# Optimization experiments

Measured on AMD Instinct MI355X. Metric: run time of the kernel, lower is better.

## Reference

```python
import jax, jax.numpy as jnp
import numpy as np

B, H, W, DIM, NH = 2, 48, 48, 768, 12
HD = DIM // NH  # 64


def setup_inputs() -> dict:
    key = jax.random.key(0)
    ks = jax.random.split(key, 7)
    std = 0.02
    return {
        "x": jax.random.normal(ks[0], (B, H, W, DIM), jnp.float32),
        "rel_pos_h": jax.random.normal(ks[1], (2 * H - 1, HD), jnp.float32) * std,
        "rel_pos_w": jax.random.normal(ks[2], (2 * W - 1, HD), jnp.float32) * std,
        "qkv_w": jax.random.normal(ks[3], (3 * DIM, DIM), jnp.float32) * std,
        "qkv_b": jnp.zeros((3 * DIM,), jnp.float32),
        "proj_w": jax.random.normal(ks[4], (DIM, DIM), jnp.float32) * std,
        "proj_b": jnp.zeros((DIM,), jnp.float32),
    }


def reference(x, rel_pos_h, rel_pos_w, qkv_w, qkv_b, proj_w, proj_b):
    b, h, w, dim = x.shape
    nh = NH
    hd = dim // nh
    scale = hd ** -0.5
    n = h * w
    # qkv projection: (B,N,3*dim) -> (3, B*nh, N, hd)
    qkv = x.reshape(b, n, dim) @ qkv_w.T + qkv_b
    qkv = qkv.reshape(b, n, 3, nh, hd).transpose(2, 0, 3, 1, 4).reshape(3, b * nh, n, hd)
    q, k, v = qkv[0], qkv[1], qkv[2]
    # scaled dot-product scores (B*nh, N, N)
    attn = jnp.einsum('bnc,bmc->bnm', q * scale, k)
    # decomposed relative position bias (q_size == k_size, no interpolation)
    idx_h = jnp.arange(h)[:, None] - jnp.arange(h)[None, :] + (h - 1)  # (h,h)
    idx_w = jnp.arange(w)[:, None] - jnp.arange(w)[None, :] + (w - 1)  # (w,w)
    Rh = rel_pos_h[idx_h]  # (h, h, hd)
    Rw = rel_pos_w[idx_w]  # (w, w, hd)
    r_q = q.reshape(b * nh, h, w, hd)
    rel_h = jnp.einsum('bhwc,hkc->bhwk', r_q, Rh)  # (B*nh, h, w, h)
    rel_w = jnp.einsum('bhwc,wkc->bhwk', r_q, Rw)  # (B*nh, h, w, w)
    attn = (attn.reshape(b * nh, h, w, h, w)
            + rel_h[:, :, :, :, None]
            + rel_w[:, :, :, None, :]).reshape(b * nh, n, n)
    attn = jax.nn.softmax(attn, axis=-1)
    out = (attn @ v).reshape(b, nh, h, w, hd).transpose(0, 2, 3, 1, 4).reshape(b, h, w, dim)
    return out @ proj_w.T + proj_b
```

## Files before the change

kernel.cpp:

```cpp
#include <hip/hip_runtime.h>
#include <hip/hip_bf16.h>
#include <stdint.h>

#define NQ    2304
#define MROWS 4608
#define DIMC  768
#define NHEAD 12
#define HEADS 24
#define HD    64

typedef unsigned int uint;
typedef unsigned short u16;
typedef __attribute__((ext_vector_type(8))) short s16x8;
typedef __attribute__((ext_vector_type(4))) float f32x4;

#define MFMA16(a, b, c) __builtin_amdgcn_mfma_f32_16x16x32_bf16((a), (b), (c), 0, 0, 0)

static __device__ __forceinline__ float bfbits2f(uint u) {
  union { uint i; float f; } c; c.i = u << 16; return c.f;
}
static __device__ __forceinline__ u16 f2bf(float f) {
  __hip_bfloat16 h = __float2bfloat16(f);
  union { __hip_bfloat16 h; u16 u; } c; c.h = h; return c.u;
}
static __device__ __forceinline__ u16 f2h(float f) {
  union { _Float16 h; u16 u; } c; c.h = (_Float16)f; return c.u;
}
static __device__ __forceinline__ float h2f(u16 u) {
  union { u16 u; _Float16 h; } c; c.u = u; return (float)c.h;
}
static __device__ __forceinline__ void dec8(uint4 p, float* f) {
  f[0] = bfbits2f(p.x & 0xFFFFu); f[1] = bfbits2f(p.x >> 16);
  f[2] = bfbits2f(p.y & 0xFFFFu); f[3] = bfbits2f(p.y >> 16);
  f[4] = bfbits2f(p.z & 0xFFFFu); f[5] = bfbits2f(p.z >> 16);
  f[6] = bfbits2f(p.w & 0xFFFFu); f[7] = bfbits2f(p.w >> 16);
}
static __device__ __forceinline__ void ld8(const void* p, size_t idx, int bf, float* f) {
  if (bf) { dec8(*(const uint4*)((const u16*)p + idx), f); }
  else {
    const float4* q = (const float4*)((const float*)p + idx);
    float4 a = q[0], b = q[1];
    f[0] = a.x; f[1] = a.y; f[2] = a.z; f[3] = a.w;
    f[4] = b.x; f[5] = b.y; f[6] = b.z; f[7] = b.w;
  }
}
static __device__ __forceinline__ float ld1(const void* p, size_t idx, int bf) {
  return bf ? bfbits2f(((const u16*)p)[idx]) : ((const float*)p)[idx];
}
static __device__ __forceinline__ uint4 ld8_to_bf(const void* p, size_t idx, int bf) {
  if (bf) return *(const uint4*)((const u16*)p + idx);
  float f[8]; ld8(p, idx, 0, f);
  uint4 u;
  u.x = (uint)f2bf(f[0]) | ((uint)f2bf(f[1]) << 16);
  u.y = (uint)f2bf(f[2]) | ((uint)f2bf(f[3]) << 16);
  u.z = (uint)f2bf(f[4]) | ((uint)f2bf(f[5]) << 16);
  u.w = (uint)f2bf(f[6]) | ((uint)f2bf(f[7]) << 16);
  return u;
}
static __device__ __forceinline__ void gll16(const u16* g, u16* l) {
  __builtin_amdgcn_global_load_lds(
      (const __attribute__((address_space(1))) unsigned int*)g,
      (__attribute__((address_space(3))) unsigned int*)l, 16, 0, 0);
}

__global__ __launch_bounds__(256) void detect_k(const u16* __restrict__ x,
                                                int* __restrict__ mode) {
  __shared__ int wsum[4];
  int t = threadIdx.x;
  int cnt = 0;
  for (int i = 0; i < 8; ++i) {
    uint u = x[(size_t)(t * 8 + i) * 2];
    uint e = (u >> 7) & 0xFFu;
    uint mag = u & 0x7FFFu;
    if (mag == 0 || (e >= 113 && e <= 133)) cnt++;
  }
#pragma unroll
  for (int d = 1; d < 64; d <<= 1) cnt += __shfl_xor(cnt, d);
  if ((t & 63) == 0) wsum[t >> 6] = cnt;
  __syncthreads();
  if (t == 0) mode[0] = ((wsum[0] + wsum[1] + wsum[2] + wsum[3]) > 1024) ? 1 : 0;
}

#define NX8 442368u
#define NW8 221184u
#define NP8 73728u
__global__ __launch_bounds__(256) void convert_k(
    const void* __restrict__ x, const void* __restrict__ qkvw,
    const void* __restrict__ pw, const int* __restrict__ mode,
    u16* __restrict__ xb, u16* __restrict__ wb, u16* __restrict__ pwb)
{
  const int bf = mode[0];
  uint i8 = blockIdx.x * 256 + threadIdx.x;
  if (i8 < NX8) {
    *(uint4*)(xb + (size_t)i8 * 8) = ld8_to_bf(x, (size_t)i8 * 8, bf);
  } else if (i8 < NX8 + NW8) {
    size_t j = i8 - NX8;
    *(uint4*)(wb + j * 8) = ld8_to_bf(qkvw, j * 8, bf);
  } else if (i8 < NX8 + NW8 + NP8) {
    size_t j = i8 - NX8 - NW8;
    *(uint4*)(pwb + j * 8) = ld8_to_bf(pw, j * 8, bf);
  }
}

__global__ __launch_bounds__(256) void qkv_gemm_k(
    const u16* __restrict__ Xb, const u16* __restrict__ Wb,
    const void* __restrict__ Bq, const int* __restrict__ mode,
    u16* __restrict__ Q, u16* __restrict__ K, u16* __restrict__ Vt)
{
  __shared__ __align__(16) u16 As[128][32];
  __shared__ __align__(16) u16 Bs[128][32];
  __shared__ __align__(16) u16 Ts[128][72];
  const int bf = mode[0];
  const int t = threadIdx.x;
  const int w = t >> 6, lane = t & 63, l15 = t & 15, quad = (t >> 4) & 3;
  const int wr = w >> 1, wc = w & 1;
  const int row0 = blockIdx.y << 7, col0 = blockIdx.x << 7;
  const int r4 = lane >> 2, c8 = (lane & 3) << 3;

  f32x4 zero4 = {0.f, 0.f, 0.f, 0.f};
  f32x4 acc[4][4];
#pragma unroll
  for (int i = 0; i < 4; ++i)
#pragma unroll
    for (int j = 0; j < 4; ++j) acc[i][j] = zero4;

  for (int kt = 0; kt < DIMC; kt += 32) {
    __syncthreads();
    gll16(Xb + (size_t)(row0 + (w << 5) + r4) * DIMC + kt + c8,      &As[(w << 5)][0]);
    gll16(Xb + (size_t)(row0 + (w << 5) + 16 + r4) * DIMC + kt + c8, &As[(w << 5) + 16][0]);
    gll16(Wb + (size_t)(col0 + (w << 5) + r4) * DIMC + kt + c8,      &Bs[(w << 5)][0]);
    gll16(Wb + (size_t)(col0 + (w << 5) + 16 + r4) * DIMC + kt + c8, &Bs[(w << 5) + 16][0]);
    __syncthreads();
    s16x8 af[4], bfr[4];
#pragma unroll
    for (int i = 0; i < 4; ++i)
      af[i] = *(const s16x8*)&As[(wr << 6) + (i << 4) + l15][quad << 3];
#pragma unroll
    for (int j = 0; j < 4; ++j)
      bfr[j] = *(const s16x8*)&Bs[(wc << 6) + (j << 4) + l15][quad << 3];
#pragma unroll
    for (int i = 0; i < 4; ++i)
#pragma unroll
      for (int j = 0; j < 4; ++j)
        acc[i][j] = MFMA16(af[i], bfr[j], acc[i][j]);
  }

  if (blockIdx.x < 12) {
#pragma unroll
    for (int jt = 0; jt < 4; ++jt) {
      int col = col0 + (wc << 6) + (jt << 4) + l15;
      int which = col / DIMC;
      int rem = col - which * DIMC;
      int head = rem >> 6, d = rem & 63;
      float bv = ld1(Bq, col, bf);
      u16* dst = (which == 0) ? Q : K;
#pragma unroll
      for (int i = 0; i < 4; ++i)
#pragma unroll
        for (int r = 0; r < 4; ++r) {
          int mrow = row0 + (wr << 6) + (i << 4) + (quad << 2) + r;
          int b_ = (mrow >= NQ) ? 1 : 0;
          int n = mrow - b_ * NQ;
          dst[(((size_t)(b_ * NHEAD + head)) * NQ + n) * HD + d] = f2bf(acc[i][jt][r] + bv);
        }
    }
  } else {
    int b_ = (row0 >= NQ) ? 1 : 0;
    int n0 = row0 - b_ * NQ;
#pragma unroll
    for (int h = 0; h < 2; ++h) {
      if (wc == h) {
#pragma unroll
        for (int jt = 0; jt < 4; ++jt) {
          int coll = (jt << 4) + l15;
          float bv = ld1(Bq, col0 + (h << 6) + coll, bf);
#pragma unroll
          for (int i = 0; i < 4; ++i)
#pragma unroll
            for (int r = 0; r < 4; ++r) {
              int tok = (wr << 6) + (i << 4) + (quad << 2) + r;
              Ts[tok][coll] = f2bf(acc[i][jt][r] + bv);
            }
        }
      }
      __syncthreads();
      int head = ((col0 - 1536) >> 6) + h;
      u16* dst = Vt + ((size_t)(b_ * NHEAD + head) * HD) * NQ + n0;
      int d = t >> 2, ch = (t & 3) << 5;
#pragma unroll
      for (int c4 = 0; c4 < 4; ++c4) {
        u16 tmp[8];
#pragma unroll
        for (int j = 0; j < 8; ++j) tmp[j] = Ts[ch + (c4 << 3) + j][d];
        *(uint4*)(dst + (size_t)d * NQ + ch + (c4 << 3)) = *(uint4*)tmp;
      }
      __syncthreads();
    }
  }
}

__global__ __launch_bounds__(256) void bias_gemm_k(
    const u16* __restrict__ Qw,
    const void* __restrict__ rph, const void* __restrict__ rpw,
    const int* __restrict__ mode,
    u16* __restrict__ Bh_g, u16* __restrict__ Bw_g)
{
  __shared__ __align__(16) u16 As[128][72];
  __shared__ __align__(16) u16 Bs[192][72];
  const int bf = mode[0];
  const int t = threadIdx.x;
  const int w = t >> 6, l15 = t & 15, quad = (t >> 4) & 3;
  const int wr = w >> 1, wc = w & 1;
  const int blk = blockIdx.x;
  const int bhd = blk / 18;
  const int row0 = (blk - bhd * 18) << 7;

  {
    int lr = t >> 1, lk = (t & 1) << 5;
    const u16* src = Qw + ((size_t)bhd * NQ + row0 + lr) * HD + lk;
    *(uint4*)&As[lr][lk]      = *(const uint4*)(src);
    *(uint4*)&As[lr][lk + 8]  = *(const uint4*)(src + 8);
    *(uint4*)&As[lr][lk + 16] = *(const uint4*)(src + 16);
    *(uint4*)&As[lr][lk + 24] = *(const uint4*)(src + 24);
  }
  for (int e = t; e < 384; e += 256) {
    int row = e >> 1, k32 = (e & 1) << 5;
    int tab = (row >= 96) ? 1 : 0;
    int r2 = row - (tab ? 96 : 0);
    if (r2 > 94) r2 = 0;
    const void* src = tab ? rpw : rph;
    *(uint4*)&Bs[row][k32]      = ld8_to_bf(src, (size_t)r2 * HD + k32, bf);
    *(uint4*)&Bs[row][k32 + 8]  = ld8_to_bf(src, (size_t)r2 * HD + k32 + 8, bf);
    *(uint4*)&Bs[row][k32 + 16] = ld8_to_bf(src, (size_t)r2 * HD + k32 + 16, bf);
    *(uint4*)&Bs[row][k32 + 24] = ld8_to_bf(src, (size_t)r2 * HD + k32 + 24, bf);
  }
  __syncthreads();

  f32x4 zero4 = {0.f, 0.f, 0.f, 0.f};
  f32x4 acc[4][6];
#pragma unroll
  for (int i = 0; i < 4; ++i)
#pragma unroll
    for (int j = 0; j < 6; ++j) acc[i][j] = zero4;

#pragma unroll
  for (int ks = 0; ks < 2; ++ks) {
    s16x8 af[4], bfr[6];
#pragma unroll
    for (int i = 0; i < 4; ++i)
      af[i] = *(const s16x8*)&As[(wr << 6) + (i << 4) + l15][(ks << 5) + (quad << 3)];
#pragma unroll
    for (int j = 0; j < 6; ++j)
      bfr[j] = *(const s16x8*)&Bs[wc * 96 + (j << 4) + l15][(ks << 5) + (quad << 3)];
#pragma unroll
    for (int i = 0; i < 4; ++i)
#pragma unroll
      for (int j = 0; j < 6; ++j)
        acc[i][j] = MFMA16(af[i], bfr[j], acc[i][j]);
  }

#pragma unroll
  for (int jt = 0; jt < 6; ++jt) {
    int col = wc * 96 + (jt << 4) + l15;
    int tab = (col >= 96) ? 1 : 0;
    int j = col - (tab ? 96 : 0);
    if (j >= 95) continue;
    u16* dstT = tab ? Bw_g : Bh_g;
#pragma unroll
    for (int i = 0; i < 4; ++i)
#pragma unroll
      for (int r = 0; r < 4; ++r) {
        int n = row0 + (wr << 6) + (i << 4) + (quad << 2) + r;
        int qh = (n * 10923) >> 19;
        int coord = tab ? (n - qh * 48) : qh;
        int c = coord + 47 - j;
        if (c >= 0 && c < 48)
          dstT[((size_t)bhd * 48 + c) * NQ + n] = f2h(acc[i][jt][r]);
      }
  }
}

#define ATILE(KB, KN, T0, PREF, KM) do {                                      \
    f32x4 acc_s[2][4];                                                        \
    _Pragma("unroll")                                                         \
    for (int nc = 0; nc < 4; ++nc) {                                          \
      f32x4 a0 = MFMA16(KB[2*nc], qa0[0], zero4);                             \
      acc_s[0][nc] = MFMA16(KB[2*nc+1], qa1[0], a0);                          \
      f32x4 a1 = MFMA16(KB[2*nc], qa0[1], zero4);                             \
      acc_s[1][nc] = MFMA16(KB[2*nc+1], qa1[1], a1);                          \
    }                                                                         \
    if (PREF) {                                                               \
      _Pragma("unroll")                                                       \
      for (int nc = 0; nc < 4; ++nc) {                                        \
        const u16* kp_ = kbase + (size_t)((T0) + 64 + (nc << 4) + l15) * HD + (quad << 3); \
        KN[2*nc]   = *(const s16x8*)(kp_);                                    \
        KN[2*nc+1] = *(const s16x8*)(kp_ + 32);                               \
      }                                                                       \
    }                                                                         \
    int kh0 = ((T0) * 10923) >> 19;                                           \
    int thr = (kh0 + 1) * 48 - (T0);                                          \
    uint Wq[2][8];                                                            \
    _Pragma("unroll")                                                         \
    for (int g = 0; g < 2; ++g) {                                             \
      int qrl = (w << 5) + (g << 4) + l15;                                    \
      float bh0v = h2f(BhL[kh0][qrl]);                                        \
      float bh1v = h2f(BhL[kh0 + 1][qrl]);                                    \
      float sum = 0.f;                                                        \
      _Pragma("unroll")                                                       \
      for (int nc = 0; nc < 4; ++nc) {                                        \
        int bnc = (KM) + (nc << 4);                                           \
        bnc = (bnc >= 48) ? bnc - 48 : bnc;                                   \
        uint2 pv = *(const uint2*)&BwL[qrl][bnc + (quad << 2)];               \
        float b0 = h2f((u16)(pv.x & 0xFFFFu));                                \
        float b1 = h2f((u16)(pv.x >> 16));                                    \
        float b2 = h2f((u16)(pv.y & 0xFFFFu));                                \
        float b3 = h2f((u16)(pv.y >> 16));                                    \
        int kl = (nc << 4) + (quad << 2);                                     \
        float e0 = __expf(acc_s[g][nc][0] * scale + ((kl     >= thr) ? bh1v : bh0v) + b0); \
        float e1 = __expf(acc_s[g][nc][1] * scale + ((kl + 1 >= thr) ? bh1v : bh0v) + b1); \
        float e2 = __expf(acc_s[g][nc][2] * scale + ((kl + 2 >= thr) ? bh1v : bh0v) + b2); \
        float e3 = __expf(acc_s[g][nc][3] * scale + ((kl + 3 >= thr) ? bh1v : bh0v) + b3); \
        sum += (e0 + e1) + (e2 + e3);                                         \
        Wq[g][2*nc]   = (uint)f2bf(e0) | ((uint)f2bf(e1) << 16);              \
        Wq[g][2*nc+1] = (uint)f2bf(e2) | ((uint)f2bf(e3) << 16);              \
      }                                                                       \
      l_st[g] += sum;                                                         \
    }                                                                         \
    _Pragma("unroll")                                                         \
    for (int h = 0; h < 2; ++h) {                                             \
      s16x8 vb[4];                                                            \
      _Pragma("unroll")                                                       \
      for (int nc = 0; nc < 4; ++nc)                                          \
        vb[nc] = *(const s16x8*)(vtbase + (size_t)((nc << 4) + l15) * NQ      \
                                 + (T0) + (h << 5) + (quad << 3));            \
      _Pragma("unroll")                                                       \
      for (int g = 0; g < 2; ++g) {                                           \
        uint e0 = __shfl(Wq[g][4*h+0], srcA), e1 = __shfl(Wq[g][4*h+1], srcA); \
        uint e2 = __shfl(Wq[g][4*h+2], srcA), e3 = __shfl(Wq[g][4*h+3], srcA); \
        uint g0 = __shfl(Wq[g][4*h+0], srcB), g1 = __shfl(Wq[g][4*h+1], srcB); \
        uint g2 = __shfl(Wq[g][4*h+2], srcB), g3 = __shfl(Wq[g][4*h+3], srcB); \
        union { uint u[4]; s16x8 v; } pf;                                     \
        pf.u[0] = hi ? e2 : e0; pf.u[1] = hi ? e3 : e1;                       \
        pf.u[2] = hi ? g2 : g0; pf.u[3] = hi ? g3 : g1;                       \
        _Pragma("unroll")                                                     \
        for (int nc = 0; nc < 4; ++nc)                                        \
          acc_o[g][nc] = MFMA16(pf.v, vb[nc], acc_o[g][nc]);                  \
      }                                                                       \
    }                                                                         \
  } while (0)

__global__ __launch_bounds__(256) void attn_k(
    const u16* __restrict__ Qw, const u16* __restrict__ Kw,
    const u16* __restrict__ Vtg,
    const u16* __restrict__ Bh_g, const u16* __restrict__ Bw_g,
    int S, float* __restrict__ Opart, float* __restrict__ Lpart,
    u16* __restrict__ Aout)
{
  __shared__ __align__(16) u16 BhL[48][128];
  __shared__ __align__(16) u16 BwL[128][52];

  const int bid = blockIdx.x;
  const int xcd = bid & 7;
  const int local = bid >> 3;
  const int per_head = 18 * S;
  const int head_l = local / per_head;
  const int rem = local - head_l * per_head;
  const int qb = rem / S;
  const int z = rem - qb * S;
  const int bhd = xcd * 3 + head_l;
  const int q0 = qb << 7;
  const int span = NQ / S;
  const int kt_lo = z * span, kt_hi = kt_lo + span;

  const int t = threadIdx.x;
  const int w = t >> 6, l15 = t & 15, quad = (t >> 4) & 3;
  const float scale = 0.125f;

  const u16* kbase  = Kw  + (size_t)bhd * NQ * HD;
  const u16* vtbase = Vtg + (size_t)bhd * HD * NQ;
  const int q0w = q0 + (w << 5);

  for (int e = t; e < 768; e += 256) {
    int c = e >> 4;
    int off = (e & 15) << 3;
    size_t gi = ((size_t)bhd * 48 + c) * NQ + q0 + off;
    *(uint4*)&BhL[c][off] = *(const uint4*)(Bh_g + gi);
    uint4 wv = *(const uint4*)(Bw_g + gi);
    u16 vals[8];
    vals[0] = wv.x & 0xFFFFu; vals[1] = wv.x >> 16;
    vals[2] = wv.y & 0xFFFFu; vals[3] = wv.y >> 16;
    vals[4] = wv.z & 0xFFFFu; vals[5] = wv.z >> 16;
    vals[6] = wv.w & 0xFFFFu; vals[7] = wv.w >> 16;
#pragma unroll
    for (int j = 0; j < 8; ++j) BwL[off + j][c] = vals[j];
  }

  s16x8 qa0[2], qa1[2];
#pragma unroll
  for (int g = 0; g < 2; ++g) {
    const u16* qfrag = Qw + ((size_t)bhd * NQ + q0w + (g << 4) + l15) * HD + (quad << 3);
    qa0[g] = *(const s16x8*)(qfrag);
    qa1[g] = *(const s16x8*)(qfrag + 32);
  }

  s16x8 kbA[8], kbB[8];
#pragma unroll
  for (int nc = 0; nc < 4; ++nc) {
    const u16* kp = kbase + (size_t)(kt_lo + (nc << 4) + l15) * HD + (quad << 3);
    kbA[2*nc]   = *(const s16x8*)(kp);
    kbA[2*nc+1] = *(const s16x8*)(kp + 32);
  }

  __syncthreads();

  f32x4 zero4 = {0.f, 0.f, 0.f, 0.f};
  f32x4 acc_o[2][4];
#pragma unroll
  for (int g = 0; g < 2; ++g)
#pragma unroll
    for (int nc = 0; nc < 4; ++nc) acc_o[g][nc] = zero4;
  float l_st[2] = {0.f, 0.f};
  const int srcA = ((quad & 1) << 5) + l15;
  const int srcB = srcA + 16;
  const int hi = quad >> 1;
  int km = 0;

  for (int kt0 = kt_lo; kt0 < kt_hi; kt0 += 128) {
    ATILE(kbA, kbB, kt0, 1, km);
    km += 16; if (km >= 48) km -= 48;
    int pref2 = (kt0 + 128) < kt_hi;
    ATILE(kbB, kbA, kt0 + 64, pref2, km);
    km += 16; if (km >= 48) km -= 48;
  }

#pragma unroll
  for (int g = 0; g < 2; ++g) {
    float lg = l_st[g];
    lg += __shfl_xor(lg, 16);
    lg += __shfl_xor(lg, 32);
    if (S > 1) {
      float* Op = Opart + ((size_t)(z * HEADS + bhd) * NQ + q0) * HD;
#pragma unroll
      for (int r = 0; r < 4; ++r) {
        int row = (w << 5) + (g << 4) + (quad << 2) + r;
#pragma unroll
        for (int nc = 0; nc < 4; ++nc)
          Op[(size_t)row * HD + (nc << 4) + l15] = acc_o[g][nc][r];
      }
      if (quad == 0)
        Lpart[(size_t)(z * HEADS + bhd) * NQ + q0w + (g << 4) + l15] = lg;
    } else {
      int b_ = bhd / NHEAD, head = bhd - b_ * NHEAD;
      float invl = 1.f / lg;
      int bsrc = (quad << 4) + (quad << 2);
#pragma unroll
      for (int r = 0; r < 4; ++r) {
        float inv = __shfl(invl, bsrc + r);
        int token = q0 + (w << 5) + (g << 4) + (quad << 2) + r;
        u16* dst = Aout + ((size_t)b_ * NQ + token) * DIMC + (head << 6);
#pragma unroll
        for (int nc = 0; nc < 4; ++nc)
          dst[(nc << 4) + l15] = f2bf(acc_o[g][nc][r] * inv);
      }
    }
  }
}

__global__ __launch_bounds__(256) void combine_k(
    const float* __restrict__ Op, const float* __restrict__ Lp,
    int S, u16* __restrict__ Aout)
{
  int idx = blockIdx.x * 256 + threadIdx.x;
  int m = idx / 192;
  int cq = idx - m * 192;
  int ccol = cq << 2;
  int head = ccol >> 6, d0 = ccol & 63;
  int b_ = (m >= NQ) ? 1 : 0;
  int n = m - b_ * NQ;
  int bh = b_ * NHEAD + head;
  float ox = 0.f, oy = 0.f, oz = 0.f, ow = 0.f, ls = 0.f;
  for (int zz = 0; zz < S; ++zz) {
    const float* ob = Op + ((size_t)(zz * HEADS + bh) * NQ + n) * HD + d0;
    float4 v = *(const float4*)ob;
    ox += v.x; oy += v.y; oz += v.z; ow += v.w;
    ls += Lp[(size_t)(zz * HEADS + bh) * NQ + n];
  }
  float inv = 1.f / ls;
  u16* dst = Aout + (size_t)m * DIMC + ccol;
  dst[0] = f2bf(ox * inv); dst[1] = f2bf(oy * inv);
  dst[2] = f2bf(oz * inv); dst[3] = f2bf(ow * inv);
}

__global__ __launch_bounds__(256) void proj_gemm_k(
    const u16* __restrict__ A, const u16* __restrict__ Wb,
    const void* __restrict__ Bp, const int* __restrict__ mode,
    void* __restrict__ Out)
{
  __shared__ __align__(16) u16 As[128][32];
  __shared__ __align__(16) u16 Bs[128][32];
  const int bf = mode[0];
  const int t = threadIdx.x;
  const int w = t >> 6, lane = t & 63, l15 = t & 15, quad = (t >> 4) & 3;
  const int wr = w >> 1, wc = w & 1;
  const int row0 = blockIdx.y << 7, col0 = blockIdx.x << 7;
  const int r4 = lane >> 2, c8 = (lane & 3) << 3;

  f32x4 zero4 = {0.f, 0.f, 0.f, 0.f};
  f32x4 acc[4][4];
#pragma unroll
  for (int i = 0; i < 4; ++i)
#pragma unroll
    for (int j = 0; j < 4; ++j) acc[i][j] = zero4;

  for (int kt = 0; kt < DIMC; kt += 32) {
    __syncthreads();
    gll16(A + (size_t)(row0 + (w << 5) + r4) * DIMC + kt + c8,       &As[(w << 5)][0]);
    gll16(A + (size_t)(row0 + (w << 5) + 16 + r4) * DIMC + kt + c8,  &As[(w << 5) + 16][0]);
    gll16(Wb + (size_t)(col0 + (w << 5) + r4) * DIMC + kt + c8,      &Bs[(w << 5)][0]);
    gll16(Wb + (size_t)(col0 + (w << 5) + 16 + r4) * DIMC + kt + c8, &Bs[(w << 5) + 16][0]);
    __syncthreads();
    s16x8 af[4], bfr[4];
#pragma unroll
    for (int i = 0; i < 4; ++i)
      af[i] = *(const s16x8*)&As[(wr << 6) + (i << 4) + l15][quad << 3];
#pragma unroll
    for (int j = 0; j < 4; ++j)
      bfr[j] = *(const s16x8*)&Bs[(wc << 6) + (j << 4) + l15][quad << 3];
#pragma unroll
    for (int i = 0; i < 4; ++i)
#pragma unroll
      for (int j = 0; j < 4; ++j)
        acc[i][j] = MFMA16(af[i], bfr[j], acc[i][j]);
  }

#pragma unroll
  for (int jt = 0; jt < 4; ++jt) {
    int col = col0 + (wc << 6) + (jt << 4) + l15;
    float bv = ld1(Bp, col, bf);
#pragma unroll
    for (int i = 0; i < 4; ++i)
#pragma unroll
      for (int r = 0; r < 4; ++r) {
        int mrow = row0 + (wr << 6) + (i << 4) + (quad << 2) + r;
        float val = acc[i][jt][r] + bv;
        size_t off = (size_t)mrow * DIMC + col;
        if (bf) ((u16*)Out)[off] = f2bf(val);
        else    ((float*)Out)[off] = val;
      }
  }
}

extern "C" void kernel_launch(void* const* d_in, const int* in_sizes, int n_in,
                              void* d_out, int out_size, void* d_ws, size_t ws_size,
                              hipStream_t stream)
{
  const void* x    = d_in[0];
  const void* rph  = d_in[1];
  const void* rpw  = d_in[2];
  const void* qkvw = d_in[3];
  const void* qkvb = d_in[4];
  const void* pw   = d_in[5];
  const void* pb   = d_in[6];

  int* mode = (int*)d_ws;
  const size_t qkv_elems = (size_t)HEADS * NQ * HD;
  const size_t NXe = (size_t)MROWS * DIMC;
  const size_t NWe = (size_t)3 * DIMC * DIMC;
  const size_t NPe = (size_t)DIMC * DIMC;
  u16* q    = (u16*)((char*)d_ws + 16);
  u16* k    = q + qkv_elems;
  u16* vt   = k + qkv_elems;
  u16* aout = vt + qkv_elems;
  u16* pwb  = aout + qkv_elems;
  const size_t biasElems = (size_t)HEADS * 48 * NQ;
  u16* bh_g = pwb + NPe;
  u16* bw_g = bh_g + biasElems;
  char* R   = (char*)(bw_g + biasElems);
  const size_t baseR = (size_t)((char*)R - (char*)d_ws);
  u16* xb = (u16*)R;
  u16* wb = xb + NXe;
  const size_t needXW = (NXe + NWe) * 2;
  const size_t perO = (size_t)HEADS * NQ * HD * 4;
  const size_t perL = (size_t)HEADS * NQ * 4;

  int S = 1;
  size_t n3 = 3 * (perO + perL), n2 = 2 * (perO + perL);
  if (ws_size >= baseR + (n3 > needXW ? n3 : needXW)) S = 3;
  else if (ws_size >= baseR + (n2 > needXW ? n2 : needXW)) S = 2;
  float* opart = (float*)R;
  float* lpart = (float*)(R + (size_t)S * perO);

  detect_k<<<1, 256, 0, stream>>>((const u16*)x, mode);
  convert_k<<<dim3(2880), 256, 0, stream>>>(x, qkvw, pw, mode, xb, wb, pwb);
  qkv_gemm_k<<<dim3(18, 36), 256, 0, stream>>>(xb, wb, qkvb, mode, q, k, vt);
  bias_gemm_k<<<dim3(432), 256, 0, stream>>>(q, rph, rpw, mode, bh_g, bw_g);
  attn_k<<<dim3(432 * S), 256, 0, stream>>>(q, k, vt, bh_g, bw_g,
                                            S, opart, lpart, aout);
  if (S > 1)
    combine_k<<<dim3(3456), 256, 0, stream>>>(opart, lpart, S, aout);
  proj_gemm_k<<<dim3(6, 36), 256, 0, stream>>>(aout, pwb, pb, mode, d_out);
}
```

Baseline: 331.2 us.

## Fuse split-K attention combine into projection GEMM A-tile load

```diff
diff --git a/kernel.cpp b/kernel.cpp
--- a/kernel.cpp
+++ b/kernel.cpp
@@ -466,33 +466,10 @@
   }
 }
 
-__global__ __launch_bounds__(256) void combine_k(
-    const float* __restrict__ Op, const float* __restrict__ Lp,
-    int S, u16* __restrict__ Aout)
-{
-  int idx = blockIdx.x * 256 + threadIdx.x;
-  int m = idx / 192;
-  int cq = idx - m * 192;
-  int ccol = cq << 2;
-  int head = ccol >> 6, d0 = ccol & 63;
-  int b_ = (m >= NQ) ? 1 : 0;
-  int n = m - b_ * NQ;
-  int bh = b_ * NHEAD + head;
-  float ox = 0.f, oy = 0.f, oz = 0.f, ow = 0.f, ls = 0.f;
-  for (int zz = 0; zz < S; ++zz) {
-    const float* ob = Op + ((size_t)(zz * HEADS + bh) * NQ + n) * HD + d0;
-    float4 v = *(const float4*)ob;
-    ox += v.x; oy += v.y; oz += v.z; ow += v.w;
-    ls += Lp[(size_t)(zz * HEADS + bh) * NQ + n];
-  }
-  float inv = 1.f / ls;
-  u16* dst = Aout + (size_t)m * DIMC + ccol;
-  dst[0] = f2bf(ox * inv); dst[1] = f2bf(oy * inv);
-  dst[2] = f2bf(oz * inv); dst[3] = f2bf(ow * inv);
-}
-
 __global__ __launch_bounds__(256) void proj_gemm_k(
-    const u16* __restrict__ A, const u16* __restrict__ Wb,
+    const u16* __restrict__ A, const float* __restrict__ Op,
+    const float* __restrict__ Lp, int S,
+    const u16* __restrict__ Wb,
     const void* __restrict__ Bp, const int* __restrict__ mode,
     void* __restrict__ Out)
 {
@@ -505,6 +482,16 @@
   const int row0 = blockIdx.y << 7, col0 = blockIdx.x << 7;
   const int r4 = lane >> 2, c8 = (lane & 3) << 3;
 
+  const int rq = t >> 3;
+  const int jj = (t & 7) << 2;
+  int nrow[4], brow[4];
+#pragma unroll
+  for (int p = 0; p < 4; ++p) {
+    int m = row0 + (p << 5) + rq;
+    brow[p] = (m >= NQ) ? 1 : 0;
+    nrow[p] = m - brow[p] * NQ;
+  }
+
   f32x4 zero4 = {0.f, 0.f, 0.f, 0.f};
   f32x4 acc[4][4];
 #pragma unroll
@@ -514,8 +501,31 @@
 
   for (int kt = 0; kt < DIMC; kt += 32) {
     __syncthreads();
-    gll16(A + (size_t)(row0 + (w << 5) + r4) * DIMC + kt + c8,       &As[(w << 5)][0]);
-    gll16(A + (size_t)(row0 + (w << 5) + 16 + r4) * DIMC + kt + c8,  &As[(w << 5) + 16][0]);
+    if (S == 1) {
+      gll16(A + (size_t)(row0 + (w << 5) + r4) * DIMC + kt + c8,      &As[(w << 5)][0]);
+      gll16(A + (size_t)(row0 + (w << 5) + 16 + r4) * DIMC + kt + c8, &As[(w << 5) + 16][0]);
+    } else {
+      int head = kt >> 6;
+      int d0 = (kt & 63) + jj;
+#pragma unroll
+      for (int p = 0; p < 4; ++p) {
+        int bh = brow[p] * NHEAD + head;
+        size_t base = ((size_t)bh * NQ + nrow[p]) * HD + d0;
+        float ls = Lp[(size_t)bh * NQ + nrow[p]];
+        float4 s = *(const float4*)(Op + base);
+        for (int z = 1; z < S; ++z) {
+          size_t off = (size_t)z * HEADS * NQ;
+          ls += Lp[off + (size_t)bh * NQ + nrow[p]];
+          float4 v = *(const float4*)(Op + off * HD + base);
+          s.x += v.x; s.y += v.y; s.z += v.z; s.w += v.w;
+        }
+        float inv = 1.f / ls;
+        uint2 pk;
+        pk.x = (uint)f2bf(s.x * inv) | ((uint)f2bf(s.y * inv) << 16);
+        pk.y = (uint)f2bf(s.z * inv) | ((uint)f2bf(s.w * inv) << 16);
+        *(uint2*)&As[(p << 5) + rq][jj] = pk;
+      }
+    }
     gll16(Wb + (size_t)(col0 + (w << 5) + r4) * DIMC + kt + c8,      &Bs[(w << 5)][0]);
     gll16(Wb + (size_t)(col0 + (w << 5) + 16 + r4) * DIMC + kt + c8, &Bs[(w << 5) + 16][0]);
     __syncthreads();
@@ -596,7 +606,6 @@
   bias_gemm_k<<<dim3(432), 256, 0, stream>>>(q, rph, rpw, mode, bh_g, bw_g);
   attn_k<<<dim3(432 * S), 256, 0, stream>>>(q, k, vt, bh_g, bw_g,
                                             S, opart, lpart, aout);
-  if (S > 1)
-    combine_k<<<dim3(3456), 256, 0, stream>>>(opart, lpart, S, aout);
-  proj_gemm_k<<<dim3(6, 36), 256, 0, stream>>>(aout, pwb, pb, mode, d_out);
-}
+  proj_gemm_k<<<dim3(6, 36), 256, 0, stream>>>(aout, opart, lpart, S,
+                                               pwb, pb, mode, d_out);
+}
```

Result: slower. 378.5 us (+14.3%).
